# Performance work log

Hardware: AMD Instinct MI355X
Metric: run time of the kernel (lower is better)

Reference implementation:

```python
import jax, jax.numpy as jnp
import numpy as np

B, C, N = 2, 512, 2048
HEADS, DIM_HEAD, SCALE = 16, 64, 8.0
H_DIM = HEADS * DIM_HEAD
EPS = 1e-12  # F.normalize default eps


def setup_inputs() -> dict:
    key = jax.random.key(0)
    ks = jax.random.split(key, 5)
    x = jax.random.normal(ks[0], (B, C, N), dtype=jnp.float32)
    Wqkv = jax.random.normal(ks[1], (3 * H_DIM, C), dtype=jnp.float32) * (1.0 / np.sqrt(C))
    q_scale = jnp.ones((DIM_HEAD,), dtype=jnp.float32)
    k_scale = jnp.ones((DIM_HEAD,), dtype=jnp.float32)
    Wout = jax.random.normal(ks[2], (C, H_DIM), dtype=jnp.float32) * (1.0 / np.sqrt(H_DIM))
    bout = jax.random.normal(ks[3], (C,), dtype=jnp.float32) * 0.01
    return {"x": x, "Wqkv": Wqkv, "q_scale": q_scale, "k_scale": k_scale,
            "Wout": Wout, "bout": bout}


def _l2norm(t):
    # F.normalize(t, dim=-1): t / max(||t||, eps)
    n = jnp.sqrt(jnp.sum(t * t, axis=-1, keepdims=True))
    return t / jnp.maximum(n, EPS)


def reference(x, Wqkv, q_scale, k_scale, Wout, bout):
    # 1x1 conv == pointwise matmul over channel dim
    qkv = jnp.einsum('oc,bcn->bon', Wqkv, x)              # [B, 3*H_DIM, N]
    q, k, v = jnp.split(qkv, 3, axis=1)
    # unflatten channels -> [B, H, D, N]
    def to_heads(t):
        return t.reshape(B, HEADS, DIM_HEAD, N)
    q, k, v = map(to_heads, (q, k, v))
    # cosine attention: l2-normalize q,k over head dim, apply learned per-dim scales
    q = _l2norm(q.transpose(0, 1, 3, 2)) * q_scale        # [B, H, N, D]
    k = _l2norm(k.transpose(0, 1, 3, 2)) * k_scale        # [B, H, N, D]
    sim = jnp.einsum('bhid,bhjd->bhij', q, k) * SCALE     # [B, H, N, N]
    attn = jax.nn.softmax(sim, axis=-1)
    out = jnp.einsum('bhij,bhdj->bhid', attn, v)          # [B, H, N, D]
    out = out.transpose(0, 1, 3, 2).reshape(B, H_DIM, N)  # b h n d -> b (h d) n
    return jnp.einsum('oc,bcn->bon', Wout, out) + bout[None, :, None]
```

## Files before the change

### kernel.cpp

```cpp
#include <hip/hip_runtime.h>
#include <hip/hip_bf16.h>

#define BATCH 2
#define CCH   512
#define NSEQ  2048
#define HEADS 16
#define DHEAD 64
#define HDIM  1024
#define ODIM  3072
#define QK_PRESCALE 11.541560327111707f

typedef short short4v __attribute__((ext_vector_type(4)));
typedef short short8 __attribute__((ext_vector_type(8)));
typedef float float4v __attribute__((ext_vector_type(4)));

__device__ __forceinline__ unsigned short f2bf(float f) {
    unsigned int u = __float_as_uint(f);
    return (unsigned short)((u + 0x7FFFu + ((u >> 16) & 1u)) >> 16);
}
__device__ __forceinline__ unsigned short f2bf_fast(float f) {
    return (unsigned short)((__float_as_uint(f) + 0x8000u) >> 16);
}
__device__ __forceinline__ float fexp2(float x) {
#if __has_builtin(__builtin_amdgcn_exp2f)
    return __builtin_amdgcn_exp2f(x);
#else
    return exp2f(x);
#endif
}

typedef __attribute__((address_space(1))) const void* as1_cvp;
typedef __attribute__((address_space(3))) void* as3_vp;
__device__ __forceinline__ void cp16(const void* g, void* l) {
    __builtin_amdgcn_global_load_lds((as1_cvp)g, (as3_vp)l, 16, 0, 0);
}

__global__ __launch_bounds__(256) void k_convert_w(
    const float* __restrict__ Wqkv, const float* __restrict__ Wout,
    const float* __restrict__ qs, const float* __restrict__ ks,
    unsigned short* __restrict__ Wqkvb, unsigned short* __restrict__ Woutb,
    float* __restrict__ M) {
    if (blockIdx.x == 0 && threadIdx.x < 64) {
        int lane = threadIdx.x;
        float p = fabsf(qs[lane] * ks[lane]);
#pragma unroll
        for (int off = 1; off < 64; off <<= 1) p = fmaxf(p, __shfl_xor(p, off));
        if (lane == 0) *M = QK_PRESCALE * p;
    }
    int i4 = (blockIdx.x * 256 + threadIdx.x) * 4;
    const float* src; unsigned short* dst; int idx;
    if (i4 < ODIM * CCH) { src = Wqkv; dst = Wqkvb; idx = i4; }
    else { src = Wout; dst = Woutb; idx = i4 - ODIM * CCH; }
    float4 v = *(const float4*)(src + idx);
    ushort4 o;
    o.x = f2bf(v.x); o.y = f2bf(v.y); o.z = f2bf(v.z); o.w = f2bf(v.w);
    *(ushort4*)(dst + idx) = o;
}

__global__ __launch_bounds__(256) void k_transpose_x(
    const float* __restrict__ x, unsigned short* __restrict__ xt) {
    __shared__ unsigned short t[64][65];
    const int b = blockIdx.z, c0 = blockIdx.y * 64, n0 = blockIdx.x * 64;
    const int tr = threadIdx.x >> 6, tc = threadIdx.x & 63;
    const float* xs = x + (size_t)b * CCH * NSEQ;
    unsigned short* xd = xt + (size_t)b * NSEQ * CCH;
#pragma unroll
    for (int r = 0; r < 16; ++r) {
        int c = r * 4 + tr;
        t[c][tc] = f2bf(xs[(size_t)(c0 + c) * NSEQ + n0 + tc]);
    }
    __syncthreads();
#pragma unroll
    for (int r = 0; r < 16; ++r) {
        int n = r * 4 + tr;
        xd[(size_t)(n0 + n) * CCH + c0 + tc] = t[tc][n];
    }
}

__global__ __launch_bounds__(256) void k_gemm_qkv(
    const unsigned short* __restrict__ W, const unsigned short* __restrict__ xt,
    const float* __restrict__ qs, const float* __restrict__ ks,
    unsigned short* __restrict__ qh, unsigned short* __restrict__ kh,
    unsigned short* __restrict__ vb) {
    constexpr int K = CCH, N = NSEQ;
    __shared__ __align__(16) short smem[2 * 128 * 64];
    short* lsA = smem;
    short* lsB = smem + 128 * 64;
    const int tid = threadIdx.x, wave = tid >> 6, lane = tid & 63;
    const int l15 = lane & 15, quad = lane >> 4;
    const int n0 = blockIdx.x * 128, m0 = blockIdx.y * 128, z = blockIdx.z;
    const short* Ab = (const short*)W + (size_t)m0 * K;
    const short* Bb = (const short*)xt + ((size_t)z * N + n0) * K;
    const int wm = wave >> 1, wn = wave & 1;
    const int cswz = (((tid & 7) ^ ((tid >> 3) & 7))) * 8;
    const int sw7 = (l15 & 7);

    float4v acc[4][4];
#pragma unroll
    for (int i = 0; i < 4; ++i)
#pragma unroll
        for (int j = 0; j < 4; ++j) acc[i][j] = (float4v){0.f, 0.f, 0.f, 0.f};

    for (int k0 = 0; k0 < K; k0 += 64) {
#pragma unroll
        for (int it = 0; it < 4; ++it) {
            int row = it * 32 + (tid >> 3);
            cp16(Ab + (size_t)row * K + k0 + cswz, &lsA[it * 2048 + wave * 512]);
            cp16(Bb + (size_t)row * K + k0 + cswz, &lsB[it * 2048 + wave * 512]);
        }
        __syncthreads();
        short8 af[4][2], bfr[4][2];
#pragma unroll
        for (int t = 0; t < 4; ++t)
#pragma unroll
            for (int kk = 0; kk < 2; ++kk) {
                af[t][kk]  = *(const short8*)&lsA[(wm * 64 + t * 16 + l15) * 64 + ((kk * 4 + quad) ^ sw7) * 8];
                bfr[t][kk] = *(const short8*)&lsB[(wn * 64 + t * 16 + l15) * 64 + ((kk * 4 + quad) ^ sw7) * 8];
            }
#pragma unroll
        for (int mt = 0; mt < 4; ++mt)
#pragma unroll
            for (int nt = 0; nt < 4; ++nt) {
                acc[mt][nt] = __builtin_amdgcn_mfma_f32_16x16x32_bf16(af[mt][0], bfr[nt][0], acc[mt][nt], 0, 0, 0);
                acc[mt][nt] = __builtin_amdgcn_mfma_f32_16x16x32_bf16(af[mt][1], bfr[nt][1], acc[mt][nt], 0, 0, 0);
            }
        __syncthreads();
    }

    const int co   = (m0 + wm * 64) >> 6;
    const int part = co >> 4;
    const int h    = co & 15;
    const int bh   = z * HEADS + h;
    short* myT = smem + wave * 4096;

    if (part < 2) {
        float inv[4];
#pragma unroll
        for (int nt = 0; nt < 4; ++nt) {
            float ss = 0.f;
#pragma unroll
            for (int mt = 0; mt < 4; ++mt)
#pragma unroll
                for (int r = 0; r < 4; ++r) ss += acc[mt][nt][r] * acc[mt][nt][r];
            ss += __shfl_xor(ss, 16);
            ss += __shfl_xor(ss, 32);
            inv[nt] = 1.0f / fmaxf(sqrtf(ss), 1e-12f);
        }
        const float* sc = part ? ks : qs;
        const float csc = part ? 1.0f : QK_PRESCALE;
#pragma unroll
        for (int mt = 0; mt < 4; ++mt) {
            const int db = mt * 16 + quad * 4;
            float4 s4 = *(const float4*)(sc + db);
            s4.x *= csc; s4.y *= csc; s4.z *= csc; s4.w *= csc;
#pragma unroll
            for (int nt = 0; nt < 4; ++nt) {
                int nl = nt * 16 + l15;
                short4v o;
                o.x = (short)f2bf(acc[mt][nt][0] * inv[nt] * s4.x);
                o.y = (short)f2bf(acc[mt][nt][1] * inv[nt] * s4.y);
                o.z = (short)f2bf(acc[mt][nt][2] * inv[nt] * s4.z);
                o.w = (short)f2bf(acc[mt][nt][3] * inv[nt] * s4.w);
                *(short4v*)&myT[nl * 64 + (((db >> 3) ^ (nl & 7)) << 3) + (db & 7)] = o;
            }
        }
        unsigned short* dst = (part ? kh : qh) + (size_t)bh * NSEQ * DHEAD
                              + (size_t)(n0 + wn * 64) * DHEAD;
#pragma unroll
        for (int pass = 0; pass < 8; ++pass) {
            int nl = pass * 8 + (lane >> 3), c = lane & 7;
            short8 vv = *(const short8*)&myT[nl * 64 + ((c ^ (nl & 7)) << 3)];
            *(short8*)&dst[(size_t)nl * DHEAD + c * 8] = vv;
        }
    } else {
#pragma unroll
        for (int mt = 0; mt < 4; ++mt)
#pragma unroll
            for (int nt = 0; nt < 4; ++nt) {
                int nl = nt * 16 + l15;
                int swc = nl >> 3, swo = nl & 7;
#pragma unroll
                for (int r = 0; r < 4; ++r) {
                    int d = mt * 16 + quad * 4 + r;
                    myT[d * 64 + ((swc ^ (d & 7)) << 3) + swo] = (short)f2bf(acc[mt][nt][r]);
                }
            }
        unsigned short* dst = vb + (size_t)bh * DHEAD * NSEQ + n0 + wn * 64;
#pragma unroll
        for (int pass = 0; pass < 8; ++pass) {
            int d = pass * 8 + (lane >> 3), c = lane & 7;
            short8 vv = *(const short8*)&myT[d * 64 + ((c ^ (d & 7)) << 3)];
            *(short8*)&dst[(size_t)d * NSEQ + c * 8] = vv;
        }
    }
}

__global__ __launch_bounds__(256, 4) void k_attn(
    const unsigned short* __restrict__ qh, const unsigned short* __restrict__ kh,
    const unsigned short* __restrict__ vb,
    float* __restrict__ opart, float* __restrict__ lpart,
    const float* __restrict__ Mptr) {
    __shared__ __align__(16) short Kt[64 * 64];
    __shared__ __align__(16) short Vt[64 * 64];
    __shared__ __align__(16) short Pt[128 * 64];
    const int tid = threadIdx.x, wave = tid >> 6, lane = tid & 63;
    const int l15 = lane & 15, quad = lane >> 4, q8 = quad * 8;
    const int flat = blockIdx.x;
    const int xcd = flat & 7, idx = flat >> 3;
    const int g = (xcd << 3) | (idx >> 4);
    const int i0 = (idx & 15) * 128;
    const int bh = g & 31, z = g >> 5;
    const float Ms = *Mptr;
    const float4v mInit = (float4v){-Ms, -Ms, -Ms, -Ms};
    const int cswz = (((tid & 7) ^ ((tid >> 3) & 7))) * 8;
    const int sw7 = (l15 & 7);

    short8 qf[2][2];
    const short* qb = (const short*)qh + ((size_t)bh * NSEQ + i0 + wave * 32) * DHEAD;
#pragma unroll
    for (int mt = 0; mt < 2; ++mt)
#pragma unroll
        for (int kt = 0; kt < 2; ++kt)
            qf[mt][kt] = *(const short8*)&qb[(mt * 16 + l15) * DHEAD + kt * 32 + q8];

    float4v of[2][4];
#pragma unroll
    for (int mt = 0; mt < 2; ++mt)
#pragma unroll
        for (int dt = 0; dt < 4; ++dt) of[mt][dt] = (float4v){0.f, 0.f, 0.f, 0.f};
    float l_acc[2][4];
#pragma unroll
    for (int mt = 0; mt < 2; ++mt)
#pragma unroll
        for (int r = 0; r < 4; ++r) l_acc[mt][r] = 0.f;

    const short* kbase = (const short*)kh + (size_t)bh * NSEQ * DHEAD;
    const short* vbase = (const short*)vb + (size_t)bh * DHEAD * NSEQ;

    const int jlo = z * (NSEQ / 2), jhi = jlo + NSEQ / 2;
    for (int j0 = jlo; j0 < jhi; j0 += 64) {
#pragma unroll
        for (int it = 0; it < 2; ++it) {
            int row = it * 32 + (tid >> 3);
            cp16(kbase + (size_t)(j0 + row) * DHEAD + cswz, &Kt[it * 2048 + wave * 512]);
            cp16(vbase + (size_t)row * NSEQ + j0 + cswz, &Vt[it * 2048 + wave * 512]);
        }
        __syncthreads();

        float4v s[2][4];
#pragma unroll
        for (int nt = 0; nt < 4; ++nt) {
            short8 kf0 = *(const short8*)&Kt[(nt * 16 + l15) * 64 + ((0 * 4 + quad) ^ sw7) * 8];
            short8 kf1 = *(const short8*)&Kt[(nt * 16 + l15) * 64 + ((1 * 4 + quad) ^ sw7) * 8];
#pragma unroll
            for (int mt = 0; mt < 2; ++mt) {
                float4v zz = mInit;
                zz = __builtin_amdgcn_mfma_f32_16x16x32_bf16(qf[mt][0], kf0, zz, 0, 0, 0);
                zz = __builtin_amdgcn_mfma_f32_16x16x32_bf16(qf[mt][1], kf1, zz, 0, 0, 0);
                s[mt][nt] = zz;
            }
        }

#pragma unroll
        for (int mt = 0; mt < 2; ++mt)
#pragma unroll
            for (int r = 0; r < 4; ++r) {
                int prow = wave * 32 + mt * 16 + quad * 4 + r;
                int psw = (prow & 7);
                float p0 = fexp2(s[mt][0][r]);
                float p1 = fexp2(s[mt][1][r]);
                float p2 = fexp2(s[mt][2][r]);
                float p3 = fexp2(s[mt][3][r]);
                l_acc[mt][r] += (p0 + p1) + (p2 + p3);
                Pt[prow * 64 + (((0 * 2 + (l15 >> 3)) ^ psw) * 8) + (l15 & 7)] = (short)f2bf_fast(p0);
                Pt[prow * 64 + (((1 * 2 + (l15 >> 3)) ^ psw) * 8) + (l15 & 7)] = (short)f2bf_fast(p1);
                Pt[prow * 64 + (((2 * 2 + (l15 >> 3)) ^ psw) * 8) + (l15 & 7)] = (short)f2bf_fast(p2);
                Pt[prow * 64 + (((3 * 2 + (l15 >> 3)) ^ psw) * 8) + (l15 & 7)] = (short)f2bf_fast(p3);
            }
        __syncthreads();

#pragma unroll
        for (int mt = 0; mt < 2; ++mt) {
            int arow = wave * 32 + mt * 16 + l15;
            short8 af0 = *(const short8*)&Pt[arow * 64 + ((0 * 4 + quad) ^ sw7) * 8];
            short8 af1 = *(const short8*)&Pt[arow * 64 + ((1 * 4 + quad) ^ sw7) * 8];
#pragma unroll
            for (int dt = 0; dt < 4; ++dt) {
                short8 vf0 = *(const short8*)&Vt[(dt * 16 + l15) * 64 + ((0 * 4 + quad) ^ sw7) * 8];
                short8 vf1 = *(const short8*)&Vt[(dt * 16 + l15) * 64 + ((1 * 4 + quad) ^ sw7) * 8];
                of[mt][dt] = __builtin_amdgcn_mfma_f32_16x16x32_bf16(af0, vf0, of[mt][dt], 0, 0, 0);
                of[mt][dt] = __builtin_amdgcn_mfma_f32_16x16x32_bf16(af1, vf1, of[mt][dt], 0, 0, 0);
            }
        }
        __syncthreads();
    }

#pragma unroll
    for (int mt = 0; mt < 2; ++mt)
#pragma unroll
        for (int r = 0; r < 4; ++r) {
            float l = l_acc[mt][r];
#pragma unroll
            for (int off = 1; off < 16; off <<= 1) l += __shfl_xor(l, off);
            l_acc[mt][r] = l;
        }

    float* ob = opart + ((size_t)(z * 32 + bh) * NSEQ) * DHEAD;
    float* lb = lpart + (size_t)(z * 32 + bh) * NSEQ;
#pragma unroll
    for (int mt = 0; mt < 2; ++mt) {
#pragma unroll
        for (int dt = 0; dt < 4; ++dt)
#pragma unroll
            for (int r = 0; r < 4; ++r) {
                int i = i0 + wave * 32 + mt * 16 + quad * 4 + r;
                ob[(size_t)i * DHEAD + dt * 16 + l15] = of[mt][dt][r];
            }
        if (l15 == 0)
#pragma unroll
            for (int r = 0; r < 4; ++r)
                lb[i0 + wave * 32 + mt * 16 + quad * 4 + r] = l_acc[mt][r];
    }
}

__global__ __launch_bounds__(256) void k_merge(
    const float* __restrict__ opart, const float* __restrict__ lpart,
    unsigned short* __restrict__ aot) {
    int t = blockIdx.x * 256 + threadIdx.x;
    int bh = t >> 15, rem = t & 32767;
    int i = rem >> 4, d = (rem & 15) * 4;
    size_t row = (size_t)bh * NSEQ + i;
    const float* o0 = opart;
    const float* o1 = opart + (size_t)32 * NSEQ * DHEAD;
    float l = lpart[row] + lpart[(size_t)32 * NSEQ + row];
    float inv = 1.0f / fmaxf(l, 1e-30f);
    float4 a = *(const float4*)(o0 + row * DHEAD + d);
    float4 b = *(const float4*)(o1 + row * DHEAD + d);
    ushort4 o;
    o.x = f2bf((a.x + b.x) * inv); o.y = f2bf((a.y + b.y) * inv);
    o.z = f2bf((a.z + b.z) * inv); o.w = f2bf((a.w + b.w) * inv);
    int bb = bh >> 4, h = bh & 15;
    *(ushort4*)(aot + ((size_t)bb * NSEQ + i) * HDIM + h * DHEAD + d) = o;
}

__global__ __launch_bounds__(256) void k_gemm_out(
    const unsigned short* __restrict__ W, const unsigned short* __restrict__ aot,
    const float* __restrict__ bias, float* __restrict__ out) {
    constexpr int K = HDIM, N = NSEQ, M = CCH;
    __shared__ __align__(16) short lsA[64 * 64];
    __shared__ __align__(16) short lsB[64 * 64];
    const int tid = threadIdx.x, wave = tid >> 6, lane = tid & 63;
    const int l15 = lane & 15, quad = lane >> 4;
    const int n0 = blockIdx.x * 64, m0 = blockIdx.y * 64, z = blockIdx.z;
    const short* Ab = (const short*)W + (size_t)m0 * K;
    const short* Bb = (const short*)aot + ((size_t)z * N + n0) * K;
    const int wm = wave >> 1, wn = wave & 1;
    const int cswz = (((tid & 7) ^ ((tid >> 3) & 7))) * 8;
    const int sw7 = (l15 & 7);

    float4v acc[2][2];
#pragma unroll
    for (int i = 0; i < 2; ++i)
#pragma unroll
        for (int j = 0; j < 2; ++j) acc[i][j] = (float4v){0.f, 0.f, 0.f, 0.f};

    for (int k0 = 0; k0 < K; k0 += 64) {
        {
            int row = tid >> 3;
            cp16(Ab + (size_t)row * K + k0 + cswz, &lsA[wave * 512]);
            cp16(Ab + (size_t)(row + 32) * K + k0 + cswz, &lsA[2048 + wave * 512]);
            cp16(Bb + (size_t)row * K + k0 + cswz, &lsB[wave * 512]);
            cp16(Bb + (size_t)(row + 32) * K + k0 + cswz, &lsB[2048 + wave * 512]);
        }
        __syncthreads();
        short8 af[2][2], bfr[2][2];
#pragma unroll
        for (int t = 0; t < 2; ++t)
#pragma unroll
            for (int kk = 0; kk < 2; ++kk) {
                af[t][kk]  = *(const short8*)&lsA[(wm * 32 + t * 16 + l15) * 64 + ((kk * 4 + quad) ^ sw7) * 8];
                bfr[t][kk] = *(const short8*)&lsB[(wn * 32 + t * 16 + l15) * 64 + ((kk * 4 + quad) ^ sw7) * 8];
            }
#pragma unroll
        for (int mt = 0; mt < 2; ++mt)
#pragma unroll
            for (int nt = 0; nt < 2; ++nt) {
                acc[mt][nt] = __builtin_amdgcn_mfma_f32_16x16x32_bf16(af[mt][0], bfr[nt][0], acc[mt][nt], 0, 0, 0);
                acc[mt][nt] = __builtin_amdgcn_mfma_f32_16x16x32_bf16(af[mt][1], bfr[nt][1], acc[mt][nt], 0, 0, 0);
            }
        __syncthreads();
    }
    float* Co = out + (size_t)z * M * N;
#pragma unroll
    for (int mt = 0; mt < 2; ++mt)
#pragma unroll
        for (int nt = 0; nt < 2; ++nt) {
            int mrow = m0 + wm * 32 + mt * 16 + quad * 4;
#pragma unroll
            for (int r = 0; r < 4; ++r) {
                int mr = mrow + r;
                int nc = n0 + wn * 32 + nt * 16 + l15;
                Co[(size_t)mr * N + nc] = acc[mt][nt][r] + bias[mr];
            }
        }
}

extern "C" void kernel_launch(void* const* d_in, const int* in_sizes, int n_in,
                              void* d_out, int out_size, void* d_ws, size_t ws_size,
                              hipStream_t stream) {
    const float* x = nullptr; const float* Wqkv = nullptr;
    const float* qs = nullptr; const float* ks = nullptr;
    const float* Wout = nullptr; const float* bout = nullptr;
    for (int i = 0; i < n_in; ++i) {
        switch (in_sizes[i]) {
            case BATCH * CCH * NSEQ: x    = (const float*)d_in[i]; break;
            case ODIM * CCH:         Wqkv = (const float*)d_in[i]; break;
            case CCH * HDIM:         Wout = (const float*)d_in[i]; break;
            case CCH:                bout = (const float*)d_in[i]; break;
            case DHEAD: if (!qs) qs = (const float*)d_in[i]; else ks = (const float*)d_in[i]; break;
            default: break;
        }
    }
    float* y = (float*)d_out;

    char* ws = (char*)d_ws;
    float*          Mbuf  = (float*)(ws + 0);
    unsigned short* Wqkvb = (unsigned short*)(ws + 4096);
    unsigned short* Woutb = (unsigned short*)(ws + 3149824);
    unsigned short* xt    = (unsigned short*)(ws + 4198400);
    unsigned short* qh    = (unsigned short*)(ws + 8392704);
    unsigned short* kh    = (unsigned short*)(ws + 16781312);
    unsigned short* vb    = (unsigned short*)(ws + 25169920);
    unsigned short* aot   = (unsigned short*)(ws + 33558528);
    float*          opart = (float*)(ws + 41947136);
    float*          lpart = (float*)(ws + 75501568);

    k_convert_w<<<(ODIM * CCH + CCH * HDIM) / 4 / 256, 256, 0, stream>>>(
        Wqkv, Wout, qs, ks, Wqkvb, Woutb, Mbuf);
    k_transpose_x<<<dim3(NSEQ / 64, CCH / 64, BATCH), 256, 0, stream>>>(x, xt);
    k_gemm_qkv<<<dim3(NSEQ / 128, ODIM / 128, BATCH), 256, 0, stream>>>(Wqkvb, xt, qs, ks, qh, kh, vb);
    k_attn<<<dim3(1024), 256, 0, stream>>>(qh, kh, vb, opart, lpart, Mbuf);
    k_merge<<<dim3(BATCH * HEADS * NSEQ * (DHEAD / 4) / 256), 256, 0, stream>>>(opart, lpart, aot);
    k_gemm_out<<<dim3(NSEQ / 64, CCH / 64, BATCH), 256, 0, stream>>>(Woutb, aot, bout, y);
}
```

Measured before the change: 176.8 us.

## Drop KV split, double-buffer K/V tiles, fuse merge into attention epilogue

The attention kernel no longer splits the key range in two. Each block now handles 64 query rows over the full sequence, with per-wave private P tiles and double-buffered K/V shared-memory tiles so the next tile's loads overlap compute. Normalization and the bf16 write into the output layout move into the attention epilogue, which removes the merge kernel and the fp32 partial-output round trip. In exchange each block does less work per K/V tile load (16 rows per wave instead of 32) and the loop chain is twice as long.

```diff
diff --git a/kernel.cpp b/kernel.cpp
--- a/kernel.cpp
+++ b/kernel.cpp
@@ -198,149 +198,113 @@
 __global__ __launch_bounds__(256, 4) void k_attn(
     const unsigned short* __restrict__ qh, const unsigned short* __restrict__ kh,
     const unsigned short* __restrict__ vb,
-    float* __restrict__ opart, float* __restrict__ lpart,
-    const float* __restrict__ Mptr) {
-    __shared__ __align__(16) short Kt[64 * 64];
-    __shared__ __align__(16) short Vt[64 * 64];
-    __shared__ __align__(16) short Pt[128 * 64];
+    unsigned short* __restrict__ aot, const float* __restrict__ Mptr) {
+    __shared__ __align__(16) short Kt[2][64 * 64];
+    __shared__ __align__(16) short Vt[2][64 * 64];
+    __shared__ __align__(16) short Pt[64 * 64];
     const int tid = threadIdx.x, wave = tid >> 6, lane = tid & 63;
     const int l15 = lane & 15, quad = lane >> 4, q8 = quad * 8;
     const int flat = blockIdx.x;
     const int xcd = flat & 7, idx = flat >> 3;
-    const int g = (xcd << 3) | (idx >> 4);
-    const int i0 = (idx & 15) * 128;
-    const int bh = g & 31, z = g >> 5;
+    const int bh = xcd * 4 + (idx >> 5);
+    const int i0 = (idx & 31) * 64;
+    const int b = bh >> 4, h = bh & 15;
     const float Ms = *Mptr;
     const float4v mInit = (float4v){-Ms, -Ms, -Ms, -Ms};
     const int cswz = (((tid & 7) ^ ((tid >> 3) & 7))) * 8;
     const int sw7 = (l15 & 7);
-
-    short8 qf[2][2];
-    const short* qb = (const short*)qh + ((size_t)bh * NSEQ + i0 + wave * 32) * DHEAD;
-#pragma unroll
-    for (int mt = 0; mt < 2; ++mt)
-#pragma unroll
-        for (int kt = 0; kt < 2; ++kt)
-            qf[mt][kt] = *(const short8*)&qb[(mt * 16 + l15) * DHEAD + kt * 32 + q8];
-
-    float4v of[2][4];
-#pragma unroll
-    for (int mt = 0; mt < 2; ++mt)
-#pragma unroll
-        for (int dt = 0; dt < 4; ++dt) of[mt][dt] = (float4v){0.f, 0.f, 0.f, 0.f};
-    float l_acc[2][4];
-#pragma unroll
-    for (int mt = 0; mt < 2; ++mt)
-#pragma unroll
-        for (int r = 0; r < 4; ++r) l_acc[mt][r] = 0.f;
+    const int srow = tid >> 3;
+
+    short8 qf[2];
+    {
+        const short* qb = (const short*)qh + ((size_t)bh * NSEQ + i0 + wave * 16) * DHEAD;
+        qf[0] = *(const short8*)&qb[l15 * DHEAD + q8];
+        qf[1] = *(const short8*)&qb[l15 * DHEAD + 32 + q8];
+    }
+
+    float4v of[4];
+#pragma unroll
+    for (int dt = 0; dt < 4; ++dt) of[dt] = (float4v){0.f, 0.f, 0.f, 0.f};
+    float l_acc[4] = {0.f, 0.f, 0.f, 0.f};
 
     const short* kbase = (const short*)kh + (size_t)bh * NSEQ * DHEAD;
     const short* vbase = (const short*)vb + (size_t)bh * DHEAD * NSEQ;
-
-    const int jlo = z * (NSEQ / 2), jhi = jlo + NSEQ / 2;
-    for (int j0 = jlo; j0 < jhi; j0 += 64) {
-#pragma unroll
-        for (int it = 0; it < 2; ++it) {
-            int row = it * 32 + (tid >> 3);
-            cp16(kbase + (size_t)(j0 + row) * DHEAD + cswz, &Kt[it * 2048 + wave * 512]);
-            cp16(vbase + (size_t)row * NSEQ + j0 + cswz, &Vt[it * 2048 + wave * 512]);
-        }
+    short* myP = Pt + wave * 1024;
+
+#pragma unroll
+    for (int it = 0; it < 2; ++it) {
+        int row = it * 32 + srow;
+        cp16(kbase + (size_t)row * DHEAD + cswz, &Kt[0][it * 2048 + wave * 512]);
+        cp16(vbase + (size_t)row * NSEQ + cswz, &Vt[0][it * 2048 + wave * 512]);
+    }
+    __syncthreads();
+
+    int buf = 0;
+    for (int j0 = 0; j0 < NSEQ; j0 += 64) {
+        if (j0 + 64 < NSEQ) {
+            int nb = buf ^ 1;
+#pragma unroll
+            for (int it = 0; it < 2; ++it) {
+                int row = it * 32 + srow;
+                cp16(kbase + (size_t)(j0 + 64 + row) * DHEAD + cswz, &Kt[nb][it * 2048 + wave * 512]);
+                cp16(vbase + (size_t)row * NSEQ + j0 + 64 + cswz, &Vt[nb][it * 2048 + wave * 512]);
+            }
+        }
+
+        float4v s[4];
+#pragma unroll
+        for (int nt = 0; nt < 4; ++nt) {
+            short8 kf0 = *(const short8*)&Kt[buf][(nt * 16 + l15) * 64 + ((0 + quad) ^ sw7) * 8];
+            short8 kf1 = *(const short8*)&Kt[buf][(nt * 16 + l15) * 64 + ((4 + quad) ^ sw7) * 8];
+            float4v zz = mInit;
+            zz = __builtin_amdgcn_mfma_f32_16x16x32_bf16(qf[0], kf0, zz, 0, 0, 0);
+            zz = __builtin_amdgcn_mfma_f32_16x16x32_bf16(qf[1], kf1, zz, 0, 0, 0);
+            s[nt] = zz;
+        }
+
+#pragma unroll
+        for (int r = 0; r < 4; ++r) {
+            int prow = quad * 4 + r;
+            int psw = prow & 7;
+            float p0 = fexp2(s[0][r]);
+            float p1 = fexp2(s[1][r]);
+            float p2 = fexp2(s[2][r]);
+            float p3 = fexp2(s[3][r]);
+            l_acc[r] += (p0 + p1) + (p2 + p3);
+            myP[prow * 64 + (((0 + (l15 >> 3)) ^ psw) * 8) + (l15 & 7)] = (short)f2bf_fast(p0);
+            myP[prow * 64 + (((2 + (l15 >> 3)) ^ psw) * 8) + (l15 & 7)] = (short)f2bf_fast(p1);
+            myP[prow * 64 + (((4 + (l15 >> 3)) ^ psw) * 8) + (l15 & 7)] = (short)f2bf_fast(p2);
+            myP[prow * 64 + (((6 + (l15 >> 3)) ^ psw) * 8) + (l15 & 7)] = (short)f2bf_fast(p3);
+        }
+
+        short8 af0 = *(const short8*)&myP[l15 * 64 + ((0 + quad) ^ sw7) * 8];
+        short8 af1 = *(const short8*)&myP[l15 * 64 + ((4 + quad) ^ sw7) * 8];
+#pragma unroll
+        for (int dt = 0; dt < 4; ++dt) {
+            short8 vf0 = *(const short8*)&Vt[buf][(dt * 16 + l15) * 64 + ((0 + quad) ^ sw7) * 8];
+            short8 vf1 = *(const short8*)&Vt[buf][(dt * 16 + l15) * 64 + ((4 + quad) ^ sw7) * 8];
+            of[dt] = __builtin_amdgcn_mfma_f32_16x16x32_bf16(af0, vf0, of[dt], 0, 0, 0);
+            of[dt] = __builtin_amdgcn_mfma_f32_16x16x32_bf16(af1, vf1, of[dt], 0, 0, 0);
+        }
+
         __syncthreads();
-
-        float4v s[2][4];
-#pragma unroll
-        for (int nt = 0; nt < 4; ++nt) {
-            short8 kf0 = *(const short8*)&Kt[(nt * 16 + l15) * 64 + ((0 * 4 + quad) ^ sw7) * 8];
-            short8 kf1 = *(const short8*)&Kt[(nt * 16 + l15) * 64 + ((1 * 4 + quad) ^ sw7) * 8];
-#pragma unroll
-            for (int mt = 0; mt < 2; ++mt) {
-                float4v zz = mInit;
-                zz = __builtin_amdgcn_mfma_f32_16x16x32_bf16(qf[mt][0], kf0, zz, 0, 0, 0);
-                zz = __builtin_amdgcn_mfma_f32_16x16x32_bf16(qf[mt][1], kf1, zz, 0, 0, 0);
-                s[mt][nt] = zz;
-            }
-        }
-
-#pragma unroll
-        for (int mt = 0; mt < 2; ++mt)
-#pragma unroll
-            for (int r = 0; r < 4; ++r) {
-                int prow = wave * 32 + mt * 16 + quad * 4 + r;
-                int psw = (prow & 7);
-                float p0 = fexp2(s[mt][0][r]);
-                float p1 = fexp2(s[mt][1][r]);
-                float p2 = fexp2(s[mt][2][r]);
-                float p3 = fexp2(s[mt][3][r]);
-                l_acc[mt][r] += (p0 + p1) + (p2 + p3);
-                Pt[prow * 64 + (((0 * 2 + (l15 >> 3)) ^ psw) * 8) + (l15 & 7)] = (short)f2bf_fast(p0);
-                Pt[prow * 64 + (((1 * 2 + (l15 >> 3)) ^ psw) * 8) + (l15 & 7)] = (short)f2bf_fast(p1);
-                Pt[prow * 64 + (((2 * 2 + (l15 >> 3)) ^ psw) * 8) + (l15 & 7)] = (short)f2bf_fast(p2);
-                Pt[prow * 64 + (((3 * 2 + (l15 >> 3)) ^ psw) * 8) + (l15 & 7)] = (short)f2bf_fast(p3);
-            }
-        __syncthreads();
-
-#pragma unroll
-        for (int mt = 0; mt < 2; ++mt) {
-            int arow = wave * 32 + mt * 16 + l15;
-            short8 af0 = *(const short8*)&Pt[arow * 64 + ((0 * 4 + quad) ^ sw7) * 8];
-            short8 af1 = *(const short8*)&Pt[arow * 64 + ((1 * 4 + quad) ^ sw7) * 8];
-#pragma unroll
-            for (int dt = 0; dt < 4; ++dt) {
-                short8 vf0 = *(const short8*)&Vt[(dt * 16 + l15) * 64 + ((0 * 4 + quad) ^ sw7) * 8];
-                short8 vf1 = *(const short8*)&Vt[(dt * 16 + l15) * 64 + ((1 * 4 + quad) ^ sw7) * 8];
-                of[mt][dt] = __builtin_amdgcn_mfma_f32_16x16x32_bf16(af0, vf0, of[mt][dt], 0, 0, 0);
-                of[mt][dt] = __builtin_amdgcn_mfma_f32_16x16x32_bf16(af1, vf1, of[mt][dt], 0, 0, 0);
-            }
-        }
-        __syncthreads();
-    }
-
-#pragma unroll
-    for (int mt = 0; mt < 2; ++mt)
-#pragma unroll
-        for (int r = 0; r < 4; ++r) {
-            float l = l_acc[mt][r];
-#pragma unroll
-            for (int off = 1; off < 16; off <<= 1) l += __shfl_xor(l, off);
-            l_acc[mt][r] = l;
-        }
-
-    float* ob = opart + ((size_t)(z * 32 + bh) * NSEQ) * DHEAD;
-    float* lb = lpart + (size_t)(z * 32 + bh) * NSEQ;
-#pragma unroll
-    for (int mt = 0; mt < 2; ++mt) {
-#pragma unroll
-        for (int dt = 0; dt < 4; ++dt)
-#pragma unroll
-            for (int r = 0; r < 4; ++r) {
-                int i = i0 + wave * 32 + mt * 16 + quad * 4 + r;
-                ob[(size_t)i * DHEAD + dt * 16 + l15] = of[mt][dt][r];
-            }
-        if (l15 == 0)
-#pragma unroll
-            for (int r = 0; r < 4; ++r)
-                lb[i0 + wave * 32 + mt * 16 + quad * 4 + r] = l_acc[mt][r];
-    }
-}
-
-__global__ __launch_bounds__(256) void k_merge(
-    const float* __restrict__ opart, const float* __restrict__ lpart,
-    unsigned short* __restrict__ aot) {
-    int t = blockIdx.x * 256 + threadIdx.x;
-    int bh = t >> 15, rem = t & 32767;
-    int i = rem >> 4, d = (rem & 15) * 4;
-    size_t row = (size_t)bh * NSEQ + i;
-    const float* o0 = opart;
-    const float* o1 = opart + (size_t)32 * NSEQ * DHEAD;
-    float l = lpart[row] + lpart[(size_t)32 * NSEQ + row];
-    float inv = 1.0f / fmaxf(l, 1e-30f);
-    float4 a = *(const float4*)(o0 + row * DHEAD + d);
-    float4 b = *(const float4*)(o1 + row * DHEAD + d);
-    ushort4 o;
-    o.x = f2bf((a.x + b.x) * inv); o.y = f2bf((a.y + b.y) * inv);
-    o.z = f2bf((a.z + b.z) * inv); o.w = f2bf((a.w + b.w) * inv);
-    int bb = bh >> 4, h = bh & 15;
-    *(ushort4*)(aot + ((size_t)bb * NSEQ + i) * HDIM + h * DHEAD + d) = o;
+        buf ^= 1;
+    }
+
+#pragma unroll
+    for (int r = 0; r < 4; ++r) {
+        float l = l_acc[r];
+        l += __shfl_xor(l, 1); l += __shfl_xor(l, 2);
+        l += __shfl_xor(l, 4); l += __shfl_xor(l, 8);
+        l_acc[r] = 1.0f / fmaxf(l, 1e-30f);
+    }
+
+    unsigned short* ob = aot + ((size_t)b * NSEQ + i0 + wave * 16) * HDIM + h * DHEAD;
+#pragma unroll
+    for (int dt = 0; dt < 4; ++dt)
+#pragma unroll
+        for (int r = 0; r < 4; ++r)
+            ob[(size_t)(quad * 4 + r) * HDIM + dt * 16 + l15] = f2bf(of[dt][r] * l_acc[r]);
 }
 
 __global__ __launch_bounds__(256) void k_gemm_out(
@@ -432,14 +396,11 @@
     unsigned short* kh    = (unsigned short*)(ws + 16781312);
     unsigned short* vb    = (unsigned short*)(ws + 25169920);
     unsigned short* aot   = (unsigned short*)(ws + 33558528);
-    float*          opart = (float*)(ws + 41947136);
-    float*          lpart = (float*)(ws + 75501568);
 
     k_convert_w<<<(ODIM * CCH + CCH * HDIM) / 4 / 256, 256, 0, stream>>>(
         Wqkv, Wout, qs, ks, Wqkvb, Woutb, Mbuf);
     k_transpose_x<<<dim3(NSEQ / 64, CCH / 64, BATCH), 256, 0, stream>>>(x, xt);
     k_gemm_qkv<<<dim3(NSEQ / 128, ODIM / 128, BATCH), 256, 0, stream>>>(Wqkvb, xt, qs, ks, qh, kh, vb);
-    k_attn<<<dim3(1024), 256, 0, stream>>>(qh, kh, vb, opart, lpart, Mbuf);
-    k_merge<<<dim3(BATCH * HEADS * NSEQ * (DHEAD / 4) / 256), 256, 0, stream>>>(opart, lpart, aot);
+    k_attn<<<dim3(1024), 256, 0, stream>>>(qh, kh, vb, aot, Mbuf);
     k_gemm_out<<<dim3(NSEQ / 64, CCH / 64, BATCH), 256, 0, stream>>>(Woutb, aot, bout, y);
 }
```

After: 171.0 us. 3.3% less time.
